# Kernel tuning notes

Hardware: AMD Instinct MI355X
Metric: run time of the kernel (lower is better)

Reference implementation:

```python
import jax, jax.numpy as jnp
import numpy as np

NBINS = 64
EPS = 1e-10
SIGMA = 1.0 / (NBINS - 1)


def setup_inputs() -> dict:
    key = jax.random.key(0)
    k1, k2 = jax.random.split(key)
    pred = jax.random.normal(k1, (8, 1, 512, 512), dtype=jnp.float32)
    target = jax.random.normal(k2, (8, 1, 512, 512), dtype=jnp.float32)
    return {"pred": pred, "target": target}


def _normalize(x):
    # per-sample min-max normalization to [0,1]
    B = x.shape[0]
    xf = x.reshape(B, -1)
    x_min = xf.min(axis=1, keepdims=True)
    x_max = xf.max(axis=1, keepdims=True)
    return (xf - x_min) / (x_max - x_min + EPS)  # (B, Npix)


def reference(pred, target):
    B = pred.shape[0]
    Npix = pred.shape[-2] * pred.shape[-1]
    centers = jnp.linspace(0.0, 1.0, NBINS, dtype=jnp.float32)  # (nbins,)

    pred_flat = _normalize(pred)      # (B, Npix)
    tgt_flat = _normalize(target)     # (B, Npix)

    inv2s2 = 1.0 / (2.0 * SIGMA * SIGMA)
    # Gaussian soft-binning weights: (B, Npix, nbins)
    w_pred = jnp.exp(-(pred_flat[:, :, None] - centers) ** 2 * inv2s2)
    w_tgt = jnp.exp(-(tgt_flat[:, :, None] - centers) ** 2 * inv2s2)

    # joint histogram via batched contraction over pixels: (B, nbins, nbins)
    p_xy = jnp.einsum('bni,bnj->bij', w_pred, w_tgt) / float(Npix)
    p_x = p_xy.sum(axis=2)  # (B, nbins)
    p_y = p_xy.sum(axis=1)  # (B, nbins)

    px_py = p_x[:, :, None] * p_y[:, None, :]
    ratio = (p_xy + EPS) / (px_py + EPS)
    mi = (p_xy * jnp.log(ratio)).sum(axis=(1, 2))  # (B,)
    return -mi.mean()
```

## Files before the change

kernel.cpp:

```cpp
#include <hip/hip_runtime.h>
#include <stdint.h>

#define NPIX  (512 * 512)
#define NB    8
#define NCH   32
#define CHPX  (NPIX / NCH)
#define FB    128
#define MPW   161
#define HDR_FLOATS 1024

typedef __attribute__((ext_vector_type(4))) unsigned uint4v;
typedef __attribute__((ext_vector_type(4))) float    float4v;

__device__ constexpr float WK[33] = {
  1.2664166e-14f, 6.1019365e-13f, 2.2897490e-11f, 6.6915858e-10f,
  1.5229979e-08f, 2.6995785e-07f, 3.7266532e-06f, 4.0065297e-05f,
  3.3546263e-04f, 2.1874911e-03f, 1.1108997e-02f, 4.3936934e-02f,
  1.3533528e-01f, 3.2465247e-01f, 6.0653066e-01f, 8.8249690e-01f,
  1.0f,
  8.8249690e-01f, 6.0653066e-01f, 3.2465247e-01f, 1.3533528e-01f,
  4.3936934e-02f, 1.1108997e-02f, 2.1874911e-03f, 3.3546263e-04f,
  4.0065297e-05f, 3.7266532e-06f, 2.6995785e-07f, 1.5229979e-08f,
  6.6915858e-10f, 2.2897490e-11f, 6.1019365e-13f, 1.2664166e-14f
};

__global__ __launch_bounds__(1024) void minmax_kernel(const float* __restrict__ pred,
                                                      const float* __restrict__ tgt,
                                                      float2* __restrict__ mm,
                                                      unsigned* __restrict__ cnt) {
  __shared__ float smin[16], smax[16];
  const int tid = threadIdx.x, lane = tid & 63, wave = tid >> 6;
  if (blockIdx.x == 0 && tid == 0) cnt[0] = 0u;
  const int pair = blockIdx.x >> 4, sub = blockIdx.x & 15;
  const float* src = pair < 8 ? pred + (size_t)pair * NPIX
                              : tgt  + (size_t)(pair - 8) * NPIX;
  const float4v* s4 = (const float4v*)src + sub * 4096;
  float vmin = 3.0e38f, vmax = -3.0e38f;
  #pragma unroll
  for (int k = 0; k < 4; ++k) {
    float4v v = s4[k * 1024 + tid];
    vmin = fminf(vmin, fminf(fminf(v[0], v[1]), fminf(v[2], v[3])));
    vmax = fmaxf(vmax, fmaxf(fmaxf(v[0], v[1]), fmaxf(v[2], v[3])));
  }
  #pragma unroll
  for (int off = 32; off; off >>= 1) {
    vmin = fminf(vmin, __shfl_xor(vmin, off));
    vmax = fmaxf(vmax, __shfl_xor(vmax, off));
  }
  if (lane == 0) { smin[wave] = vmin; smax[wave] = vmax; }
  __syncthreads();
  if (tid == 0) {
    float m = smin[0], M = smax[0];
    #pragma unroll
    for (int w = 1; w < 16; ++w) { m = fminf(m, smin[w]); M = fmaxf(M, smax[w]); }
    mm[blockIdx.x] = (float2){m, M};
  }
}

__global__ __launch_bounds__(512) void fine_hist_kernel(const float* __restrict__ pred,
                                                        const float* __restrict__ tgt,
                                                        const float2* __restrict__ mm,
                                                        unsigned* __restrict__ part) {
  __shared__ unsigned H[FB * FB / 2];
  const int tid = threadIdx.x;
  const int b = blockIdx.x >> 5, c = blockIdx.x & 31;

  float pmin = 3.0e38f, pmax = -3.0e38f, tmin = 3.0e38f, tmax = -3.0e38f;
  #pragma unroll
  for (int s2 = 0; s2 < 16; ++s2) {
    float2 a = mm[b * 16 + s2], d = mm[(8 + b) * 16 + s2];
    pmin = fminf(pmin, a.x); pmax = fmaxf(pmax, a.y);
    tmin = fminf(tmin, d.x); tmax = fmaxf(tmax, d.y);
  }
  const float sp = 126.0f / (pmax - pmin + 1e-10f), op = -pmin * sp + 0.5f;
  const float st = 126.0f / (tmax - tmin + 1e-10f), ot = -tmin * st + 0.5f;

  #pragma unroll
  for (int j = 0; j < 4; ++j)
    ((uint4v*)H)[j * 512 + tid] = (uint4v){0u, 0u, 0u, 0u};
  __syncthreads();

  const float4v* p4 = (const float4v*)(pred + (size_t)b * NPIX + (size_t)c * CHPX);
  const float4v* t4 = (const float4v*)(tgt  + (size_t)b * NPIX + (size_t)c * CHPX);
  #pragma unroll
  for (int it = 0; it < 4; ++it) {
    float4v vp = p4[it * 512 + tid];
    float4v vt = t4[it * 512 + tid];
    #pragma unroll
    for (int j = 0; j < 4; ++j) {
      int fp = (int)(vp[j] * sp + op);
      int ft = (int)(vt[j] * st + ot);
      int w  = (fp << 6) | (ft >> 1);
      atomicAdd(&H[w ^ ((fp & 7) << 2)], 1u << ((ft & 1) << 4));
    }
  }
  __syncthreads();

  uint4v* dst = (uint4v*)(part + ((size_t)blockIdx.x << 13));
  #pragma unroll
  for (int j = 0; j < 4; ++j) {
    int g = j * 512 + tid;
    dst[g] = ((uint4v*)H)[g ^ ((g >> 4) & 7)];
  }
}

__global__ __launch_bounds__(256) void reduce_fine_kernel(const unsigned* __restrict__ part,
                                                          float2* __restrict__ fineF) {
  const int tid = threadIdx.x;
  const int b = blockIdx.x >> 5, sl = blockIdx.x & 31;
  const int w = sl * 256 + tid;
  const unsigned* src = part + ((size_t)b << 18) + w;
  unsigned lo = 0, hi = 0;
  #pragma unroll 8
  for (int c = 0; c < 32; ++c) {
    unsigned v = src[(size_t)c << 13];
    lo += v & 0xFFFFu; hi += v >> 16;
  }
  float2 o; o.x = (float)lo; o.y = (float)hi;
  fineF[(size_t)b * 8192 + w] = o;
}

__global__ __launch_bounds__(1024) void tail_kernel(const float* __restrict__ fineG,
                                                    float* __restrict__ mi,
                                                    unsigned* __restrict__ cnt,
                                                    float* __restrict__ out) {
  __shared__ float S[14608];
  const int tid = threadIdx.x, lane = tid & 63, wave = tid >> 6;
  const int b = blockIdx.x;

  {
    const int ft = tid & 127, r = tid >> 7;
    const float* fb = fineG + ((size_t)b << 14) + ft;
    float v[47];
    #pragma unroll
    for (int t = 0; t < 47; ++t) {
      int fp = 16 * r - 16 + t;
      v[t] = ((unsigned)fp < 128u) ? fb[fp << 7] : 0.0f;
    }
    float acc[8];
    #pragma unroll
    for (int d = 0; d < 8; ++d) {
      float a = 0.0f;
      #pragma unroll
      for (int k = 0; k < 33; ++k) a += WK[k] * v[2 * d + k];
      acc[d] = a;
    }
    #pragma unroll
    for (int d = 0; d < 8; ++d)
      S[(8 * r + d) * MPW + ft + 16] = acc[d];
    #pragma unroll
    for (int ii = 0; ii < 3; ++ii) {
      int idx = ii * 1024 + tid;
      if (idx < 64 * 33) {
        int rr = idx / 33, cc = idx % 33;
        int col = cc < 16 ? cc : cc + 128;
        S[rr * MPW + col] = 0.0f;
      }
    }
  }
  __syncthreads();

  const int i = tid & 63, js = (tid >> 6) << 2;
  {
    float v[39];
    #pragma unroll
    for (int t = 0; t < 39; ++t) v[t] = S[i * MPW + 2 * js + t];
    float acc[4] = {0.0f, 0.0f, 0.0f, 0.0f};
    #pragma unroll
    for (int d = 0; d < 4; ++d)
      #pragma unroll
      for (int k = 0; k < 33; ++k) acc[d] += WK[k] * v[2 * d + k];
    const float invN = 1.0f / (float)NPIX;
    #pragma unroll
    for (int d = 0; d < 4; ++d) S[10304 + i * 65 + js + d] = acc[d] * invN;
  }
  __syncthreads();

  {
    const int l16 = lane & 15, sub16 = lane >> 4;
    int row = 4 * wave + sub16;
    float s = 0.0f;
    #pragma unroll
    for (int k = 0; k < 4; ++k) s += S[10304 + row * 65 + l16 * 4 + k];
    #pragma unroll
    for (int off = 8; off; off >>= 1) s += __shfl_xor(s, off);
    if (l16 == 0) S[14464 + row] = s;
    float t2 = 0.0f;
    #pragma unroll
    for (int k = 0; k < 4; ++k) t2 += S[10304 + (l16 * 4 + k) * 65 + row];
    #pragma unroll
    for (int off = 8; off; off >>= 1) t2 += __shfl_xor(t2, off);
    if (l16 == 0) S[14528 + row] = t2;
  }
  __syncthreads();

  float a = 0.0f;
  #pragma unroll
  for (int r = 0; r < 4; ++r) {
    int e = r * 1024 + tid;
    int ii = e >> 6, jj = e & 63;
    float pv = S[10304 + ii * 65 + jj];
    float d = S[14464 + ii] * S[14528 + jj] + 1e-10f;
    a += pv * __logf((pv + 1e-10f) / d);
  }
  #pragma unroll
  for (int off = 32; off; off >>= 1) a += __shfl_xor(a, off);
  if (lane == 0) S[14592 + wave] = a;
  __syncthreads();

  if (tid == 0) {
    float s = 0.0f;
    #pragma unroll
    for (int w = 0; w < 16; ++w) s += S[14592 + w];
    atomicExch(&mi[b], s);
    __threadfence();
    unsigned prev = atomicAdd(cnt, 1u);
    if (prev == NB - 1) {
      __threadfence();
      float tot = 0.0f;
      #pragma unroll
      for (int k = 0; k < NB; ++k) tot += atomicAdd(&mi[k], 0.0f);
      out[0] = -(tot * (1.0f / NB));
      atomicExch(cnt, 0u);
    }
  }
}

extern "C" void kernel_launch(void* const* d_in, const int* in_sizes, int n_in,
                              void* d_out, int out_size, void* d_ws, size_t ws_size,
                              hipStream_t stream) {
  const float* pred = (const float*)d_in[0];
  const float* tgt  = (const float*)d_in[1];
  float*    out  = (float*)d_out;
  float*    wsf  = (float*)d_ws;
  float2*   mm   = (float2*)d_ws;
  float*    mi   = wsf + 512;
  unsigned* cnt  = (unsigned*)(wsf + 520);
  unsigned* part = (unsigned*)(wsf + HDR_FLOATS);
  float*    fineG = wsf + HDR_FLOATS + (size_t)NB * NCH * 8192;

  minmax_kernel     <<<256,      1024, 0, stream>>>(pred, tgt, mm, cnt);
  fine_hist_kernel  <<<NB * NCH,  512, 0, stream>>>(pred, tgt, mm, part);
  reduce_fine_kernel<<<256,       256, 0, stream>>>(part, (float2*)fineG);
  tail_kernel       <<<NB,       1024, 0, stream>>>(fineG, mi, cnt, out);
}
```

Baseline: 29.32 us.

## Merge fine histogram partials with global atomics, drop reduction kernel

Each histogram block now adds its nonzero 16-bit packed bin counts straight into a per-batch global fine histogram with atomicAdd, skipping empty bins. This removes the partial-histogram buffer write and the separate reduction kernel launch. The global histogram is zeroed inside the min/max kernel, and the tail kernel reads unsigned counts directly. The cost is contended global atomics from 32 blocks per batch on the same cells.

```diff
diff --git a/kernel.cpp b/kernel.cpp
--- a/kernel.cpp
+++ b/kernel.cpp
@@ -27,10 +27,13 @@
 __global__ __launch_bounds__(1024) void minmax_kernel(const float* __restrict__ pred,
                                                       const float* __restrict__ tgt,
                                                       float2* __restrict__ mm,
+                                                      unsigned* __restrict__ fineW,
                                                       unsigned* __restrict__ cnt) {
   __shared__ float smin[16], smax[16];
   const int tid = threadIdx.x, lane = tid & 63, wave = tid >> 6;
-  if (blockIdx.x == 0 && tid == 0) cnt[0] = 0u;
+  if (blockIdx.x == 0 && tid < 4) cnt[tid] = 0u;
+  if (tid < 128)
+    ((uint4v*)fineW)[blockIdx.x * 128 + tid] = (uint4v){0u, 0u, 0u, 0u};
   const int pair = blockIdx.x >> 4, sub = blockIdx.x & 15;
   const float* src = pair < 8 ? pred + (size_t)pair * NPIX
                               : tgt  + (size_t)(pair - 8) * NPIX;
@@ -60,7 +63,7 @@
 __global__ __launch_bounds__(512) void fine_hist_kernel(const float* __restrict__ pred,
                                                         const float* __restrict__ tgt,
                                                         const float2* __restrict__ mm,
-                                                        unsigned* __restrict__ part) {
+                                                        unsigned* __restrict__ fineW) {
   __shared__ unsigned H[FB * FB / 2];
   const int tid = threadIdx.x;
   const int b = blockIdx.x >> 5, c = blockIdx.x & 31;
@@ -96,31 +99,21 @@
   }
   __syncthreads();
 
-  uint4v* dst = (uint4v*)(part + ((size_t)blockIdx.x << 13));
-  #pragma unroll
-  for (int j = 0; j < 4; ++j) {
-    int g = j * 512 + tid;
-    dst[g] = ((uint4v*)H)[g ^ ((g >> 4) & 7)];
-  }
-}
-
-__global__ __launch_bounds__(256) void reduce_fine_kernel(const unsigned* __restrict__ part,
-                                                          float2* __restrict__ fineF) {
-  const int tid = threadIdx.x;
-  const int b = blockIdx.x >> 5, sl = blockIdx.x & 31;
-  const int w = sl * 256 + tid;
-  const unsigned* src = part + ((size_t)b << 18) + w;
-  unsigned lo = 0, hi = 0;
-  #pragma unroll 8
-  for (int c = 0; c < 32; ++c) {
-    unsigned v = src[(size_t)c << 13];
-    lo += v & 0xFFFFu; hi += v >> 16;
-  }
-  float2 o; o.x = (float)lo; o.y = (float)hi;
-  fineF[(size_t)b * 8192 + w] = o;
-}
-
-__global__ __launch_bounds__(1024) void tail_kernel(const float* __restrict__ fineG,
+  unsigned* fw = fineW + ((size_t)b << 14);
+  #pragma unroll
+  for (int j = 0; j < 16; ++j) {
+    int w = j * 512 + tid;
+    unsigned v = H[w ^ (((w >> 6) & 7) << 2)];
+    if (v) {
+      int cell = ((w >> 6) << 7) | ((w & 63) << 1);
+      unsigned lo = v & 0xFFFFu, hi = v >> 16;
+      if (lo) atomicAdd(&fw[cell], lo);
+      if (hi) atomicAdd(&fw[cell + 1], hi);
+    }
+  }
+}
+
+__global__ __launch_bounds__(1024) void tail_kernel(const unsigned* __restrict__ fineW,
                                                     float* __restrict__ mi,
                                                     unsigned* __restrict__ cnt,
                                                     float* __restrict__ out) {
@@ -130,12 +123,12 @@
 
   {
     const int ft = tid & 127, r = tid >> 7;
-    const float* fb = fineG + ((size_t)b << 14) + ft;
+    const unsigned* fb = fineW + ((size_t)b << 14) + ft;
     float v[47];
     #pragma unroll
     for (int t = 0; t < 47; ++t) {
       int fp = 16 * r - 16 + t;
-      v[t] = ((unsigned)fp < 128u) ? fb[fp << 7] : 0.0f;
+      v[t] = ((unsigned)fp < 128u) ? (float)fb[fp << 7] : 0.0f;
     }
     float acc[8];
     #pragma unroll
@@ -236,11 +229,9 @@
   float2*   mm   = (float2*)d_ws;
   float*    mi   = wsf + 512;
   unsigned* cnt  = (unsigned*)(wsf + 520);
-  unsigned* part = (unsigned*)(wsf + HDR_FLOATS);
-  float*    fineG = wsf + HDR_FLOATS + (size_t)NB * NCH * 8192;
-
-  minmax_kernel     <<<256,      1024, 0, stream>>>(pred, tgt, mm, cnt);
-  fine_hist_kernel  <<<NB * NCH,  512, 0, stream>>>(pred, tgt, mm, part);
-  reduce_fine_kernel<<<256,       256, 0, stream>>>(part, (float2*)fineG);
-  tail_kernel       <<<NB,       1024, 0, stream>>>(fineG, mi, cnt, out);
-}
+  unsigned* fineW = (unsigned*)(wsf + HDR_FLOATS);
+
+  minmax_kernel   <<<256,      1024, 0, stream>>>(pred, tgt, mm, fineW, cnt);
+  fine_hist_kernel<<<NB * NCH,  512, 0, stream>>>(pred, tgt, mm, fineW);
+  tail_kernel     <<<NB,       1024, 0, stream>>>(fineW, mi, cnt, out);
+}
```

New measurement: 38.35 us. 30.8% more time.
